# Kernel tuning notes

Measured on AMD Instinct MI355X. Metric: run time of the kernel, lower is better.

Reference implementation:

```python
import jax, jax.numpy as jnp
import numpy as np


def setup_inputs() -> dict:
    key = jax.random.key(0)
    k1, k2 = jax.random.split(key)
    E, D1, D2 = 512, 4096, 16
    # Center row scaled up, error rows scaled down so lb/ub straddle 0 for a
    # realistic mix of dead / stable-positive / crossing neurons.
    center = jax.random.normal(k1, (1, D1, D2), dtype=jnp.float32) * 3.0
    errs = jax.random.normal(k2, (E - 1, D1, D2), dtype=jnp.float32) * 0.01
    x = jnp.concatenate([center, errs], axis=0)
    return {"x": x}


def reference(x):
    size = x.shape
    E = size[0]
    N = int(np.prod(size[1:]))
    xf = x.reshape(E, N)  # [error_terms, neurons]

    # zonotope bounds
    sum_abs = jnp.sum(jnp.abs(xf[1:]), axis=0)  # [N]
    lb = xf[0] - sum_abs
    ub = xf[0] + sum_abs

    crossing = (lb <= 0) & (ub >= 0)  # neurons needing relaxation
    dead = ub <= 0                    # neurons fully zeroed

    # Faithful to source bug: alpha = ub/ub - lb == 1 - lb (missing parens),
    # valid whenever ub != 0 on crossing neurons (a.s. with float data).
    alpha = jnp.where(crossing, 1.0 - lb, 1.0)  # [N]

    center = jnp.where(crossing, alpha * xf[0] - alpha * lb * 0.5, xf[0])
    rest = jnp.where(crossing[None, :], alpha[None, :] * xf[1:], xf[1:])
    out = jnp.concatenate([center[None, :], rest], axis=0)  # [E, N]

    # zero out columns with ub <= 0 (applied after the crossing update,
    # matching the source's statement order)
    out = jnp.where(dead[None, :], 0.0, out)

    # Source's `if new_error_terms.size():` is always truthy -> same shape out.
    return out.reshape(size)
```

## Files before the change

kernel.cpp:

```cpp
#include <hip/hip_runtime.h>


#define EROWS 512
#define W4 8
#define BLK 256
#define ROWS_PER_ITER (BLK / W4)
#define NITER (EROWS / ROWS_PER_ITER)

__global__ __launch_bounds__(BLK) void ar_fused(const float* __restrict__ x,
                                                float* __restrict__ out, int n4) {
    __shared__ float4 slab[EROWS * W4];
    __shared__ float4 part[BLK];
    __shared__ float4 scale4[W4];

    int t = threadIdx.x;
    int cseg  = t & (W4 - 1);
    int rbase = t >> 3;
    int col4_0 = blockIdx.x * W4;

    const float4* xv = (const float4*)x;
    float4* ov = (float4*)out;

    float4 acc = {0.f, 0.f, 0.f, 0.f};
    {
        float4 v = xv[(size_t)rbase * n4 + col4_0 + cseg];
        slab[rbase * W4 + cseg] = v;
        if (rbase != 0) {
            acc.x += fabsf(v.x); acc.y += fabsf(v.y);
            acc.z += fabsf(v.z); acc.w += fabsf(v.w);
        }
    }
    #pragma unroll
    for (int k = 1; k < NITER; ++k) {
        int row = rbase + k * ROWS_PER_ITER;
        float4 v = xv[(size_t)row * n4 + col4_0 + cseg];
        slab[row * W4 + cseg] = v;
        acc.x += fabsf(v.x); acc.y += fabsf(v.y);
        acc.z += fabsf(v.z); acc.w += fabsf(v.w);
    }
    part[t] = acc;
    __syncthreads();

    if (t < W4) {
        float4 s = {0.f, 0.f, 0.f, 0.f};
        for (int j = 0; j < ROWS_PER_ITER; ++j) {
            float4 p = part[j * W4 + t];
            s.x += p.x; s.y += p.y; s.z += p.z; s.w += p.w;
        }
        float4 x0v = slab[t];
        float x0[4] = {x0v.x, x0v.y, x0v.z, x0v.w};
        float sm[4] = {s.x, s.y, s.z, s.w};
        float sc[4], o0[4];
        #pragma unroll
        for (int j = 0; j < 4; ++j) {
            float lb = x0[j] - sm[j];
            float ub = x0[j] + sm[j];
            bool crossing = (lb <= 0.f) && (ub >= 0.f);
            bool dead = (ub <= 0.f);
            float alpha = crossing ? (1.f - lb) : 1.f;
            float scl = dead ? 0.f : (crossing ? alpha : 1.f);
            float addv = (crossing && !dead) ? (-alpha * lb * 0.5f) : 0.f;
            sc[j] = scl;
            o0[j] = scl * x0[j] + addv;
        }
        float4 scv = {sc[0], sc[1], sc[2], sc[3]};
        float4 o0v = {o0[0], o0[1], o0[2], o0[3]};
        scale4[t] = scv;
        ov[col4_0 + t] = o0v;
    }
    __syncthreads();

    for (int i = W4 + t; i < EROWS * W4; i += BLK) {
        int row = i >> 3;
        int cs  = i & (W4 - 1);
        float4 v = slab[i];
        float4 s = scale4[cs];
        float4 o;
        o.x = v.x * s.x; o.y = v.y * s.y;
        o.z = v.z * s.z; o.w = v.w * s.w;
        ov[(size_t)row * n4 + col4_0 + cs] = o;
    }
}

extern "C" void kernel_launch(void* const* d_in, const int* in_sizes, int n_in,
                              void* d_out, int out_size, void* d_ws, size_t ws_size,
                              hipStream_t stream) {
    const float* x = (const float*)d_in[0];
    float* out = (float*)d_out;
    int total = in_sizes[0];
    int N = total / EROWS;
    int n4 = N >> 2;
    int nblocks = n4 / W4;

    ar_fused<<<nblocks, BLK, 0, stream>>>(x, out, n4);
}
```

Before: 45.67 us.

## Keep column slab in registers instead of shared memory

Each thread now loads its 16 float4 rows into a register array and reuses them for both the abs-sum reduction and the scaled write-back, eliminating the 64KB shared-memory slab. This removes LDS stores/loads and lifts the LDS-imposed occupancy limit, with launch bounds requesting 4 blocks per CU. The cost is higher VGPR pressure, which could cause spills or limit occupancy differently.

```diff
diff --git a/kernel.cpp b/kernel.cpp
--- a/kernel.cpp
+++ b/kernel.cpp
@@ -4,51 +4,49 @@
 #define EROWS 512
 #define W4 8
 #define BLK 256
-#define ROWS_PER_ITER (BLK / W4)
-#define NITER (EROWS / ROWS_PER_ITER)
+#define RSTRIDE (BLK / W4)
+#define RPT (EROWS / RSTRIDE)
 
-__global__ __launch_bounds__(BLK) void ar_fused(const float* __restrict__ x,
-                                                float* __restrict__ out, int n4) {
-    __shared__ float4 slab[EROWS * W4];
+__global__ __launch_bounds__(BLK, 4) void ar_fused(const float* __restrict__ x,
+                                                   float* __restrict__ out, int n4) {
     __shared__ float4 part[BLK];
     __shared__ float4 scale4[W4];
 
     int t = threadIdx.x;
     int cseg  = t & (W4 - 1);
     int rbase = t >> 3;
-    int col4_0 = blockIdx.x * W4;
+    int col4 = blockIdx.x * W4 + cseg;
 
     const float4* xv = (const float4*)x;
     float4* ov = (float4*)out;
 
-    float4 acc = {0.f, 0.f, 0.f, 0.f};
-    {
-        float4 v = xv[(size_t)rbase * n4 + col4_0 + cseg];
-        slab[rbase * W4 + cseg] = v;
-        if (rbase != 0) {
-            acc.x += fabsf(v.x); acc.y += fabsf(v.y);
-            acc.z += fabsf(v.z); acc.w += fabsf(v.w);
-        }
+    float4 v[RPT];
+    #pragma unroll
+    for (int k = 0; k < RPT; ++k)
+        v[k] = xv[(size_t)(rbase + k * RSTRIDE) * n4 + col4];
+
+    float4 acc;
+    if (rbase == 0) {
+        acc.x = 0.f; acc.y = 0.f; acc.z = 0.f; acc.w = 0.f;
+    } else {
+        acc.x = fabsf(v[0].x); acc.y = fabsf(v[0].y);
+        acc.z = fabsf(v[0].z); acc.w = fabsf(v[0].w);
     }
     #pragma unroll
-    for (int k = 1; k < NITER; ++k) {
-        int row = rbase + k * ROWS_PER_ITER;
-        float4 v = xv[(size_t)row * n4 + col4_0 + cseg];
-        slab[row * W4 + cseg] = v;
-        acc.x += fabsf(v.x); acc.y += fabsf(v.y);
-        acc.z += fabsf(v.z); acc.w += fabsf(v.w);
+    for (int k = 1; k < RPT; ++k) {
+        acc.x += fabsf(v[k].x); acc.y += fabsf(v[k].y);
+        acc.z += fabsf(v[k].z); acc.w += fabsf(v[k].w);
     }
     part[t] = acc;
     __syncthreads();
 
     if (t < W4) {
         float4 s = {0.f, 0.f, 0.f, 0.f};
-        for (int j = 0; j < ROWS_PER_ITER; ++j) {
+        for (int j = 0; j < RSTRIDE; ++j) {
             float4 p = part[j * W4 + t];
             s.x += p.x; s.y += p.y; s.z += p.z; s.w += p.w;
         }
-        float4 x0v = slab[t];
-        float x0[4] = {x0v.x, x0v.y, x0v.z, x0v.w};
+        float x0[4] = {v[0].x, v[0].y, v[0].z, v[0].w};
         float sm[4] = {s.x, s.y, s.z, s.w};
         float sc[4], o0[4];
         #pragma unroll
@@ -66,19 +64,23 @@
         float4 scv = {sc[0], sc[1], sc[2], sc[3]};
         float4 o0v = {o0[0], o0[1], o0[2], o0[3]};
         scale4[t] = scv;
-        ov[col4_0 + t] = o0v;
+        ov[col4] = o0v;
     }
     __syncthreads();
 
-    for (int i = W4 + t; i < EROWS * W4; i += BLK) {
-        int row = i >> 3;
-        int cs  = i & (W4 - 1);
-        float4 v = slab[i];
-        float4 s = scale4[cs];
+    float4 s = scale4[cseg];
+    if (rbase != 0) {
         float4 o;
-        o.x = v.x * s.x; o.y = v.y * s.y;
-        o.z = v.z * s.z; o.w = v.w * s.w;
-        ov[(size_t)row * n4 + col4_0 + cs] = o;
+        o.x = v[0].x * s.x; o.y = v[0].y * s.y;
+        o.z = v[0].z * s.z; o.w = v[0].w * s.w;
+        ov[(size_t)rbase * n4 + col4] = o;
+    }
+    #pragma unroll
+    for (int k = 1; k < RPT; ++k) {
+        float4 o;
+        o.x = v[k].x * s.x; o.y = v[k].y * s.y;
+        o.z = v[k].z * s.z; o.w = v[k].w * s.w;
+        ov[(size_t)(rbase + k * RSTRIDE) * n4 + col4] = o;
     }
 }
 
```

Result: slower. 58.74 us (+28.6%).

## Drop shared-memory slab and re-read input from global in scale pass

Applied to the files above, without the earlier changes.

Removes the 64KB LDS slab that held the block's whole column tile. The scale pass now re-reads x from global memory, relying on L2 or the MI355X's large last-level cache to serve the reload. The per-thread partial sums are reduced with wave shuffles instead of a 256-entry LDS array. Freeing LDS should allow more resident blocks per CU, at the cost of reading the input twice from global memory.

```diff
diff --git a/kernel.cpp b/kernel.cpp
--- a/kernel.cpp
+++ b/kernel.cpp
@@ -4,50 +4,51 @@
 #define EROWS 512
 #define W4 8
 #define BLK 256
-#define ROWS_PER_ITER (BLK / W4)
-#define NITER (EROWS / ROWS_PER_ITER)
+#define RSTRIDE (BLK / W4)
+#define RPT (EROWS / RSTRIDE)
+#define NWAVES (BLK / 64)
 
 __global__ __launch_bounds__(BLK) void ar_fused(const float* __restrict__ x,
                                                 float* __restrict__ out, int n4) {
-    __shared__ float4 slab[EROWS * W4];
-    __shared__ float4 part[BLK];
+    __shared__ float4 part[NWAVES][W4];
     __shared__ float4 scale4[W4];
 
     int t = threadIdx.x;
     int cseg  = t & (W4 - 1);
     int rbase = t >> 3;
-    int col4_0 = blockIdx.x * W4;
+    int col4 = blockIdx.x * W4 + cseg;
 
     const float4* xv = (const float4*)x;
     float4* ov = (float4*)out;
 
     float4 acc = {0.f, 0.f, 0.f, 0.f};
-    {
-        float4 v = xv[(size_t)rbase * n4 + col4_0 + cseg];
-        slab[rbase * W4 + cseg] = v;
-        if (rbase != 0) {
+    #pragma unroll
+    for (int k = 0; k < RPT; ++k) {
+        int row = rbase + k * RSTRIDE;
+        float4 v = xv[(size_t)row * n4 + col4];
+        if (row != 0) {
             acc.x += fabsf(v.x); acc.y += fabsf(v.y);
             acc.z += fabsf(v.z); acc.w += fabsf(v.w);
         }
     }
     #pragma unroll
-    for (int k = 1; k < NITER; ++k) {
-        int row = rbase + k * ROWS_PER_ITER;
-        float4 v = xv[(size_t)row * n4 + col4_0 + cseg];
-        slab[row * W4 + cseg] = v;
-        acc.x += fabsf(v.x); acc.y += fabsf(v.y);
-        acc.z += fabsf(v.z); acc.w += fabsf(v.w);
+    for (int d = W4; d < 64; d <<= 1) {
+        acc.x += __shfl_xor(acc.x, d);
+        acc.y += __shfl_xor(acc.y, d);
+        acc.z += __shfl_xor(acc.z, d);
+        acc.w += __shfl_xor(acc.w, d);
     }
-    part[t] = acc;
+    if ((t & 63) < W4) part[t >> 6][cseg] = acc;
     __syncthreads();
 
     if (t < W4) {
         float4 s = {0.f, 0.f, 0.f, 0.f};
-        for (int j = 0; j < ROWS_PER_ITER; ++j) {
-            float4 p = part[j * W4 + t];
+        #pragma unroll
+        for (int w = 0; w < NWAVES; ++w) {
+            float4 p = part[w][t];
             s.x += p.x; s.y += p.y; s.z += p.z; s.w += p.w;
         }
-        float4 x0v = slab[t];
+        float4 x0v = xv[blockIdx.x * W4 + t];
         float x0[4] = {x0v.x, x0v.y, x0v.z, x0v.w};
         float sm[4] = {s.x, s.y, s.z, s.w};
         float sc[4], o0[4];
@@ -66,19 +67,20 @@
         float4 scv = {sc[0], sc[1], sc[2], sc[3]};
         float4 o0v = {o0[0], o0[1], o0[2], o0[3]};
         scale4[t] = scv;
-        ov[col4_0 + t] = o0v;
+        ov[blockIdx.x * W4 + t] = o0v;
     }
     __syncthreads();
 
-    for (int i = W4 + t; i < EROWS * W4; i += BLK) {
-        int row = i >> 3;
-        int cs  = i & (W4 - 1);
-        float4 v = slab[i];
-        float4 s = scale4[cs];
+    float4 s = scale4[cseg];
+    #pragma unroll
+    for (int k = 0; k < RPT; ++k) {
+        int row = rbase + k * RSTRIDE;
+        if (row == 0) continue;
+        float4 v = xv[(size_t)row * n4 + col4];
         float4 o;
         o.x = v.x * s.x; o.y = v.y * s.y;
         o.z = v.z * s.z; o.w = v.w * s.w;
-        ov[(size_t)row * n4 + col4_0 + cs] = o;
+        ov[(size_t)row * n4 + col4] = o;
     }
 }
 
```

New measurement: 64.49 us. +41.2%, slower.
